# Optimization experiments

Hardware: AMD Instinct MI355X
Metric: run time of the kernel (lower is better)

Reference implementation:

```python
import jax, jax.numpy as jnp
import numpy as np

B, S, D_IN = 16, 4096, 1024
H, HD = 8, 64            # num_heads, head_dim
V = H * HD               # value_dim = 512
F_OUT = 120              # forecast_horizon
EPS = 1e-5


def _rotate(x):
    # theta_shift in the source ignores sin/cos: stack((-x2, x1)) and flatten
    x1 = x[..., 0::2]
    x2 = x[..., 1::2]
    return jnp.stack((-x2, x1), axis=-1).reshape(x.shape)


def setup_inputs() -> dict:
    key = jax.random.key(0)
    kx, kq, kk, kv, ko, _ = jax.random.split(key, 6)
    return {
        "x": jax.random.normal(kx, (B, S, D_IN), dtype=jnp.float32),
        "Wq": jax.random.normal(kq, (V, D_IN), dtype=jnp.float32) * 0.02,
        "Wk": jax.random.normal(kk, (V, D_IN), dtype=jnp.float32) * 0.02,
        "Wv": jax.random.normal(kv, (V, D_IN), dtype=jnp.float32) * 0.02,
        "Wout": jax.random.normal(ko, (F_OUT, V), dtype=jnp.float32) * 0.02,
        "gamma": jnp.ones((V,), dtype=jnp.float32),  # RMSNorm weight
    }


def reference(x, Wq, Wk, Wv, Wout, gamma):
    b, s, _ = x.shape
    scaling = HD ** -0.5
    q = (x @ Wq.T) * scaling          # [B,S,V]
    k = (x @ Wk.T) * scaling
    v = (x @ Wv.T).reshape(b, H, s, HD)   # raw view reinterpretation (as in torch)
    qr = _rotate(q).reshape(b, H, s, HD)  # raw view, matches torch .view
    kr = _rotate(k).reshape(b, H, s, HD)
    # recurrent_forward with incremental_state=None:
    # kv = 0.9*0 + 0.1*(kr*v); output = sum_s(qr*kv); scale = S
    kv = 0.1 * (kr * v)
    out = jnp.sum(qr * kv, axis=2) / jnp.float32(s)  # [B,H,HD]
    out = out.reshape(b, H * HD)                      # [B,V]
    # RMSNorm
    rms = out * jax.lax.rsqrt(jnp.mean(out * out, axis=-1, keepdims=True) + EPS) * gamma
    g = jax.nn.gelu(rms, approximate=False)  # torch F.gelu default = exact erf
    return g @ Wout.T                         # [B, forecast_horizon]
```

## Files before the change

### kernel.cpp

```cpp
#include <hip/hip_runtime.h>
#include <hip/hip_bf16.h>
#include <math.h>

#define B_   16
#define S_   4096
#define DIN  1024
#define V_   512
#define FOUT 120

typedef __attribute__((ext_vector_type(8))) short bf16x8;
typedef __attribute__((ext_vector_type(4))) float f32x4;

#define AS1 __attribute__((address_space(1)))
#define AS3 __attribute__((address_space(3)))

__device__ const float CSCALE = 0.1f / (64.0f * 4096.0f);
__device__ const float EPSF = 1e-5f;

__device__ inline void gl2lds16(const void* g, void* l) {
  __builtin_amdgcn_global_load_lds((const AS1 unsigned int*)g,
                                   (AS3 unsigned int*)l, 16, 0, 0);
}

__device__ inline unsigned short f2b(float f) {
  unsigned u = __builtin_bit_cast(unsigned, f);
  unsigned r = (u + 0x7FFFu + ((u >> 16) & 1u)) >> 16;
  return (unsigned short)r;
}

__device__ inline bf16x8 pack8(float4 a, float4 b) {
  bf16x8 r;
  r[0] = (short)f2b(a.x); r[1] = (short)f2b(a.y);
  r[2] = (short)f2b(a.z); r[3] = (short)f2b(a.w);
  r[4] = (short)f2b(b.x); r[5] = (short)f2b(b.y);
  r[6] = (short)f2b(b.z); r[7] = (short)f2b(b.w);
  return r;
}

template <bool DOX>
__global__ __launch_bounds__(256) void msr_conv(
    const float* __restrict__ Wq, const float* __restrict__ Wk,
    const float* __restrict__ Wv, const float* __restrict__ x,
    unsigned short* __restrict__ Wt, unsigned short* __restrict__ Xb,
    float* __restrict__ outacc) {
  const int bid = blockIdx.x;
  if (bid < 768) {
    int e = bid * 256 + threadIdx.x;
    int l = e & 63;
    int f = (e >> 6) % 24;
    int ck = (e >> 6) / 24;
    int k = ck & 31;
    int ct = ck >> 5;
    int nf = f / 3, g = f % 3;
    const float* W = (g == 0) ? Wq : (g == 1) ? Wk : Wv;
    int ch = ct * 128 + nf * 16 + (l & 15);
    const float* src = W + (size_t)ch * DIN + k * 32 + (l >> 4) * 8;
    float4 a = *(const float4*)src;
    float4 b = *(const float4*)(src + 4);
    *(bf16x8*)(Wt + (size_t)e * 8) = pack8(a, b);
  } else if (DOX && bid < 2816) {
    const size_t stride = 2048ull * 256;
    for (size_t i = (size_t)(bid - 768) * 256 + threadIdx.x; i < 8388608ull; i += stride) {
      const float* src = x + i * 8;
      float4 a = *(const float4*)src;
      float4 b = *(const float4*)(src + 4);
      *(bf16x8*)(Xb + i * 8) = pack8(a, b);
    }
  } else {
    for (int i = threadIdx.x; i < B_ * V_; i += 256) outacc[i] = 0.f;
  }
}

#define WAITVM5  asm volatile("s_waitcnt vmcnt(5)" ::: "memory")
#define WAITVM3  asm volatile("s_waitcnt vmcnt(3)" ::: "memory")
#define WAITVM0  asm volatile("s_waitcnt vmcnt(0)" ::: "memory")
#define WAITLGKM asm volatile("s_waitcnt lgkmcnt(0)" ::: "memory")
#define SCHEDB   __builtin_amdgcn_sched_barrier(0)
#define BARRIER  { asm volatile("" ::: "memory"); __builtin_amdgcn_s_barrier(); asm volatile("" ::: "memory"); }

template <bool DIRECT>
__global__ __launch_bounds__(512, 2) void msr_main(
    const float* __restrict__ x, const unsigned short* __restrict__ Xb,
    const unsigned short* __restrict__ Wt, float* __restrict__ outacc) {
  const int bid = blockIdx.x;
  const int xcd = bid & 7;
  const int j = bid >> 3;
  const int ct = j & 3;
  const int rt = xcd * 32 + (j >> 2);
  const int r0 = rt << 8;

  __shared__ __align__(16) unsigned char smem_[122880];

  const int t = threadIdx.x;
  const int w = t >> 6, lane = t & 63;
  const int l16 = lane * 16;
  const int w3 = w * 3;
  const int ctk = ct * 32;
  const int amb = (w >> 2) * 8192;
  const int bread = 16384 + 6 * (w & 3) * 1024 + l16;

  const unsigned short* srcA0 =
      Xb + (size_t)(r0 + w * 16 + (lane & 15)) * DIN + ((lane >> 4) << 3);
  const unsigned short* srcA1 = srcA0 + (size_t)128 * DIN;
  const float* pXf = x + (size_t)(r0 + w * 16 + (lane & 15)) * DIN + ((lane >> 4) << 3);

  f32x4 acc[3][8][2];
#pragma unroll
  for (int g = 0; g < 3; ++g)
#pragma unroll
    for (int m = 0; m < 8; ++m)
#pragma unroll
      for (int n = 0; n < 2; ++n) acc[g][m][n] = (f32x4){0.f, 0.f, 0.f, 0.f};

#define STAGE(KK, SB) { \
  unsigned char* _sb = smem_ + (SB) * 40960; \
  if constexpr (DIRECT) { \
    gl2lds16(srcA0 + (size_t)(KK) * 32, _sb + w * 1024); \
    gl2lds16(srcA1 + (size_t)(KK) * 32, _sb + (8 + w) * 1024); \
  } else { \
    const float* _p0 = pXf + (size_t)(KK) * 32; \
    const float* _p1 = _p0 + (size_t)128 * DIN; \
    *(bf16x8*)(_sb + (w * 64 + lane) * 16) = \
        pack8(*(const float4*)_p0, *(const float4*)(_p0 + 4)); \
    *(bf16x8*)(_sb + ((8 + w) * 64 + lane) * 16) = \
        pack8(*(const float4*)_p1, *(const float4*)(_p1 + 4)); \
  } \
  _Pragma("unroll") for (int i = 0; i < 3; ++i) \
    gl2lds16(Wt + ((size_t)(ctk + (KK)) * 24 + w3 + i) * 512 + (size_t)lane * 8, \
             _sb + 16384 + (w3 + i) * 1024); }

#define COMPUTE(KB) { \
  const unsigned char* _kb = smem_ + (KB) * 40960; \
  bf16x8 _bfr[6]; \
  _Pragma("unroll") for (int i = 0; i < 6; ++i) \
    _bfr[i] = *(const bf16x8*)(_kb + bread + i * 1024); \
  __builtin_amdgcn_s_setprio(1); \
  _Pragma("unroll") for (int m = 0; m < 8; ++m) { \
    bf16x8 _afr = *(const bf16x8*)(_kb + amb + m * 1024 + l16); \
    _Pragma("unroll") for (int g = 0; g < 3; ++g) { \
      acc[g][m][0] = __builtin_amdgcn_mfma_f32_16x16x32_bf16(_afr, _bfr[g],     acc[g][m][0], 0, 0, 0); \
      acc[g][m][1] = __builtin_amdgcn_mfma_f32_16x16x32_bf16(_afr, _bfr[3 + g], acc[g][m][1], 0, 0, 0); \
    } \
  } \
  __builtin_amdgcn_s_setprio(0); }

#define STEP(KB, SB, KK, DOSTAGE, VMD, VMF) { \
  if (DOSTAGE) { STAGE((KK) + 2, SB); } \
  SCHEDB; \
  COMPUTE(KB); \
  if constexpr (DIRECT) { VMD; } else { WAITLGKM; VMF; } \
  BARRIER; }

  STAGE(0, 0);
  STAGE(1, 1);
  if constexpr (DIRECT) { WAITVM5; } else { WAITLGKM; WAITVM3; }
  BARRIER;

#pragma unroll 1
  for (int i = 0; i < 10; ++i) {
    const int k3 = i * 3;
    STEP(0, 2, k3,     1, WAITVM5, WAITVM3);
    STEP(1, 0, k3 + 1, 1, WAITVM5, WAITVM3);
    STEP(2, 1, k3 + 2, 1, WAITVM5, WAITVM3);
  }
  STEP(0, 0, 30, 0, WAITVM0, WAITVM0);
  COMPUTE(1);
#undef STEP
#undef COMPUTE
#undef STAGE

  float pd0 = 0.f, pd1 = 0.f;
#pragma unroll
  for (int m = 0; m < 8; ++m)
#pragma unroll
    for (int r = 0; r < 4; ++r) {
      float qk0 = acc[0][m][0][r] * acc[1][m][0][r];
      float qk1 = acc[0][m][1][r] * acc[1][m][1][r];
      pd0 += __shfl_xor(qk0, 1, 64) * acc[2][m][0][r];
      pd1 += __shfl_xor(qk1, 1, 64) * acc[2][m][1][r];
    }
  pd0 += __shfl_xor(pd0, 16, 64); pd0 += __shfl_xor(pd0, 32, 64);
  pd1 += __shfl_xor(pd1, 16, 64); pd1 += __shfl_xor(pd1, 32, 64);

  if (lane < 16) {
    float* dst = &outacc[((rt >> 1) << 6) + (w & 1) * 32 + lane];
    atomicAdd(dst, pd0);
    atomicAdd(dst + 16, pd1);
  }
}

__global__ __launch_bounds__(256) void msr_finish(
    const float* __restrict__ outacc, const float* __restrict__ gamma,
    const float* __restrict__ Wout, float* __restrict__ y) {
  const int b = blockIdx.x;
  const int t = threadIdx.x;
  __shared__ float g[V_];
  __shared__ float wsum[4];

  float v0 = outacc[b * V_ + t] * CSCALE;
  float v1 = outacc[b * V_ + 256 + t] * CSCALE;
  float ss = v0 * v0 + v1 * v1;
#pragma unroll
  for (int o = 32; o > 0; o >>= 1) ss += __shfl_down(ss, o, 64);
  if ((t & 63) == 0) wsum[t >> 6] = ss;
  __syncthreads();
  float tot = wsum[0] + wsum[1] + wsum[2] + wsum[3];
  float rs = rsqrtf(tot * (1.0f / (float)V_) + EPSF);

  float r0v = v0 * rs * gamma[t];
  float r1v = v1 * rs * gamma[t + 256];
  g[t]       = 0.5f * r0v * (1.0f + erff(r0v * 0.70710678118654752f));
  g[t + 256] = 0.5f * r1v * (1.0f + erff(r1v * 0.70710678118654752f));
  __syncthreads();

  if (t < FOUT) {
    const float* wr = Wout + (size_t)t * V_;
    float acc = 0.f;
#pragma unroll 4
    for (int c = 0; c < V_; c += 4) {
      float4 w4 = *(const float4*)(wr + c);
      acc += g[c] * w4.x + g[c + 1] * w4.y + g[c + 2] * w4.z + g[c + 3] * w4.w;
    }
    y[b * FOUT + t] = acc;
  }
}

extern "C" void kernel_launch(void* const* d_in, const int* in_sizes, int n_in,
                              void* d_out, int out_size, void* d_ws, size_t ws_size,
                              hipStream_t stream) {
  const float* x     = (const float*)d_in[0];
  const float* Wq    = (const float*)d_in[1];
  const float* Wk    = (const float*)d_in[2];
  const float* Wv    = (const float*)d_in[3];
  const float* Wout  = (const float*)d_in[4];
  const float* gamma = (const float*)d_in[5];

  float* outacc = (float*)d_ws;
  unsigned short* Wt = (unsigned short*)((char*)d_ws + 32768);
  unsigned short* Xb = (unsigned short*)((char*)d_ws + 32768 + 3145728);
  float* y = (float*)d_out;

  const size_t need = 32768ull + 3145728ull + 134217728ull;

  if (ws_size >= need) {
    msr_conv<true><<<2817, 256, 0, stream>>>(Wq, Wk, Wv, x, Wt, Xb, outacc);
    msr_main<true><<<1024, 512, 0, stream>>>(x, Xb, Wt, outacc);
  } else {
    msr_conv<false><<<769, 256, 0, stream>>>(Wq, Wk, Wv, x, Wt, Xb, outacc);
    msr_main<false><<<1024, 512, 0, stream>>>(x, Xb, Wt, outacc);
  }
  msr_finish<<<B_, 256, 0, stream>>>(outacc, gamma, Wout, y);
}
```

Measured before the change: 244.6 us.

## Switch fused QKV GEMM from 16x16x32 to 32x32x16 MFMA tiles

Replaces the 16x16x32 bf16 MFMA tiling with 32x32x16 MFMA instructions. The weight pre-layout, the LDS staging of X rows, the fragment reads and the epilogue reduction are all reorganised to match the new 32-row, 32-column fragments. Each wave now owns 32 consecutive rows and does fewer, larger MFMAs with fewer A-fragment LDS reads per output. The aim is higher MFMA efficiency and less LDS traffic, but the new layout changes LDS bank access patterns and accumulator register usage.

```diff
diff --git a/kernel.cpp b/kernel.cpp
--- a/kernel.cpp
+++ b/kernel.cpp
@@ -9,7 +9,7 @@
 #define FOUT 120
 
 typedef __attribute__((ext_vector_type(8))) short bf16x8;
-typedef __attribute__((ext_vector_type(4))) float f32x4;
+typedef __attribute__((ext_vector_type(16))) float f32x16;
 
 #define AS1 __attribute__((address_space(1)))
 #define AS3 __attribute__((address_space(3)))
@@ -51,10 +51,12 @@
     int ck = (e >> 6) / 24;
     int k = ck & 31;
     int ct = ck >> 5;
-    int nf = f / 3, g = f % 3;
+    int kh = f / 12;
+    int nf = (f % 12) / 3;
+    int g = f % 3;
     const float* W = (g == 0) ? Wq : (g == 1) ? Wk : Wv;
-    int ch = ct * 128 + nf * 16 + (l & 15);
-    const float* src = W + (size_t)ch * DIN + k * 32 + (l >> 4) * 8;
+    int ch = ct * 128 + nf * 32 + (l & 31);
+    const float* src = W + (size_t)ch * DIN + k * 32 + kh * 16 + (l >> 5) * 8;
     float4 a = *(const float4*)src;
     float4 b = *(const float4*)(src + 4);
     *(bf16x8*)(Wt + (size_t)e * 8) = pack8(a, b);
@@ -96,33 +98,32 @@
   const int l16 = lane * 16;
   const int w3 = w * 3;
   const int ctk = ct * 32;
-  const int amb = (w >> 2) * 8192;
-  const int bread = 16384 + 6 * (w & 3) * 1024 + l16;
+  const int amb = (w >> 2) * 4096;
+  const int bread0 = 16384 + (w & 3) * 3 * 1024 + l16;
 
   const unsigned short* srcA0 =
-      Xb + (size_t)(r0 + w * 16 + (lane & 15)) * DIN + ((lane >> 4) << 3);
-  const unsigned short* srcA1 = srcA0 + (size_t)128 * DIN;
-  const float* pXf = x + (size_t)(r0 + w * 16 + (lane & 15)) * DIN + ((lane >> 4) << 3);
-
-  f32x4 acc[3][8][2];
+      Xb + (size_t)(r0 + w * 32 + (lane & 31)) * DIN + ((lane >> 5) << 3);
+  const float* pXf = x + (size_t)(r0 + w * 32 + (lane & 31)) * DIN + ((lane >> 5) << 3);
+
+  f32x16 acc[3][4];
 #pragma unroll
   for (int g = 0; g < 3; ++g)
 #pragma unroll
-    for (int m = 0; m < 8; ++m)
-#pragma unroll
-      for (int n = 0; n < 2; ++n) acc[g][m][n] = (f32x4){0.f, 0.f, 0.f, 0.f};
+    for (int m = 0; m < 4; ++m)
+#pragma unroll
+      for (int r = 0; r < 16; ++r) acc[g][m][r] = 0.f;
 
 #define STAGE(KK, SB) { \
   unsigned char* _sb = smem_ + (SB) * 40960; \
   if constexpr (DIRECT) { \
     gl2lds16(srcA0 + (size_t)(KK) * 32, _sb + w * 1024); \
-    gl2lds16(srcA1 + (size_t)(KK) * 32, _sb + (8 + w) * 1024); \
+    gl2lds16(srcA0 + (size_t)(KK) * 32 + 16, _sb + (8 + w) * 1024); \
   } else { \
     const float* _p0 = pXf + (size_t)(KK) * 32; \
-    const float* _p1 = _p0 + (size_t)128 * DIN; \
-    *(bf16x8*)(_sb + (w * 64 + lane) * 16) = \
+    const float* _p1 = _p0 + 16; \
+    *(bf16x8*)(_sb + w * 1024 + l16) = \
         pack8(*(const float4*)_p0, *(const float4*)(_p0 + 4)); \
-    *(bf16x8*)(_sb + ((8 + w) * 64 + lane) * 16) = \
+    *(bf16x8*)(_sb + (8 + w) * 1024 + l16) = \
         pack8(*(const float4*)_p1, *(const float4*)(_p1 + 4)); \
   } \
   _Pragma("unroll") for (int i = 0; i < 3; ++i) \
@@ -132,15 +133,17 @@
 #define COMPUTE(KB) { \
   const unsigned char* _kb = smem_ + (KB) * 40960; \
   bf16x8 _bfr[6]; \
-  _Pragma("unroll") for (int i = 0; i < 6; ++i) \
-    _bfr[i] = *(const bf16x8*)(_kb + bread + i * 1024); \
+  _Pragma("unroll") for (int kh = 0; kh < 2; ++kh) \
+    _Pragma("unroll") for (int g = 0; g < 3; ++g) \
+      _bfr[kh * 3 + g] = *(const bf16x8*)(_kb + bread0 + (kh * 12 + g) * 1024); \
   __builtin_amdgcn_s_setprio(1); \
-  _Pragma("unroll") for (int m = 0; m < 8; ++m) { \
-    bf16x8 _afr = *(const bf16x8*)(_kb + amb + m * 1024 + l16); \
-    _Pragma("unroll") for (int g = 0; g < 3; ++g) { \
-      acc[g][m][0] = __builtin_amdgcn_mfma_f32_16x16x32_bf16(_afr, _bfr[g],     acc[g][m][0], 0, 0, 0); \
-      acc[g][m][1] = __builtin_amdgcn_mfma_f32_16x16x32_bf16(_afr, _bfr[3 + g], acc[g][m][1], 0, 0, 0); \
-    } \
+  _Pragma("unroll") for (int m = 0; m < 4; ++m) { \
+    bf16x8 _a0 = *(const bf16x8*)(_kb + amb + m * 1024 + l16); \
+    bf16x8 _a1 = *(const bf16x8*)(_kb + 8192 + amb + m * 1024 + l16); \
+    _Pragma("unroll") for (int g = 0; g < 3; ++g) \
+      acc[g][m] = __builtin_amdgcn_mfma_f32_32x32x16_bf16(_a0, _bfr[g], acc[g][m], 0, 0, 0); \
+    _Pragma("unroll") for (int g = 0; g < 3; ++g) \
+      acc[g][m] = __builtin_amdgcn_mfma_f32_32x32x16_bf16(_a1, _bfr[3 + g], acc[g][m], 0, 0, 0); \
   } \
   __builtin_amdgcn_s_setprio(0); }
 
@@ -169,23 +172,18 @@
 #undef COMPUTE
 #undef STAGE
 
-  float pd0 = 0.f, pd1 = 0.f;
-#pragma unroll
-  for (int m = 0; m < 8; ++m)
-#pragma unroll
-    for (int r = 0; r < 4; ++r) {
-      float qk0 = acc[0][m][0][r] * acc[1][m][0][r];
-      float qk1 = acc[0][m][1][r] * acc[1][m][1][r];
-      pd0 += __shfl_xor(qk0, 1, 64) * acc[2][m][0][r];
-      pd1 += __shfl_xor(qk1, 1, 64) * acc[2][m][1][r];
+  float pd = 0.f;
+#pragma unroll
+  for (int m = 0; m < 4; ++m)
+#pragma unroll
+    for (int r = 0; r < 16; ++r) {
+      float qk = acc[0][m][r] * acc[1][m][r];
+      pd += __shfl_xor(qk, 1, 64) * acc[2][m][r];
     }
-  pd0 += __shfl_xor(pd0, 16, 64); pd0 += __shfl_xor(pd0, 32, 64);
-  pd1 += __shfl_xor(pd1, 16, 64); pd1 += __shfl_xor(pd1, 32, 64);
-
-  if (lane < 16) {
-    float* dst = &outacc[((rt >> 1) << 6) + (w & 1) * 32 + lane];
-    atomicAdd(dst, pd0);
-    atomicAdd(dst + 16, pd1);
+  pd += __shfl_xor(pd, 32, 64);
+
+  if (lane < 32) {
+    atomicAdd(&outacc[((rt >> 1) << 6) + (w & 1) * 32 + lane], pd);
   }
 }
 
```

Measured after the change: 281.1 us. 1.15x slower.
